# Performance work log

Hardware: AMD Instinct MI355X
Metric: run time of the kernel (lower is better)

The kernel has to match this reference:

```python
import jax, jax.numpy as jnp
import numpy as np

B, T, D = 2, 2048, 1024
H, C = 16, 64  # num_heads, head_dim
ROPE_BASE = 10000.0


def _rope(x):
    # x: [b, h, t, c]; standard rotate-half RoPE over the head dim
    t, c = x.shape[2], x.shape[3]
    inv_freq = 1.0 / (ROPE_BASE ** (jnp.arange(0, c, 2, dtype=jnp.float32) / c))  # [c/2]
    angles = jnp.arange(t, dtype=jnp.float32)[:, None] * inv_freq[None, :]        # [t, c/2]
    cos = jnp.concatenate([jnp.cos(angles), jnp.cos(angles)], axis=-1)            # [t, c]
    sin = jnp.concatenate([jnp.sin(angles), jnp.sin(angles)], axis=-1)            # [t, c]
    x1, x2 = x[..., : c // 2], x[..., c // 2 :]
    rot = jnp.concatenate([-x2, x1], axis=-1)
    return x * cos + rot * sin


def setup_inputs() -> dict:
    key = jax.random.key(0)
    ks = jax.random.split(key, 7)
    s_in = 1.0 / np.sqrt(D)
    s_attn = 1.0 / np.sqrt(H * C)
    return {
        "x": jax.random.normal(ks[0], (B, T, D), dtype=jnp.float32),
        "Wq": jax.random.normal(ks[1], (D, H * C), dtype=jnp.float32) * s_in,
        "bq": jnp.zeros((H * C,), dtype=jnp.float32),
        "Wkv": jax.random.normal(ks[2], (D, 2 * H * C), dtype=jnp.float32) * s_in,
        "bkv": jnp.zeros((2 * H * C,), dtype=jnp.float32),
        "Wo": jax.random.normal(ks[3], (H * C, D), dtype=jnp.float32) * s_attn,
        "bo": jnp.zeros((D,), dtype=jnp.float32),
    }


def reference(x, Wq, bq, Wkv, bkv, Wo, bo):
    b, t, _ = x.shape
    q = x @ Wq + bq                                  # [b, t, h*c]
    kv = x @ Wkv + bkv                               # [b, t, 2*h*c]
    k, v = jnp.split(kv, 2, axis=-1)
    # 'b t (h c) -> b h t c'
    to_heads = lambda z: z.reshape(b, t, H, C).transpose(0, 2, 1, 3)
    q, k, v = to_heads(q), to_heads(k), to_heads(v)
    q = _rope(q)
    k = _rope(k)
    scale = 1.0 / jnp.sqrt(jnp.asarray(C, dtype=q.dtype))
    scores = jnp.einsum("bhtc,bhsc->bhts", q, k) * scale   # [b, h, t, t]
    attn = jax.nn.softmax(scores, axis=-1)
    out = jnp.einsum("bhts,bhsc->bhtc", attn, v)            # [b, h, t, c]
    out = out.transpose(0, 2, 1, 3).reshape(b, t, H * C)    # 'b h t c -> b t (h c)'
    return out @ Wo + bo
```

## Files before the change

kernel.cpp:

```cpp
#include <hip/hip_runtime.h>
#include <hip/hip_bf16.h>
#include <math.h>


typedef _Float16 half8 __attribute__((ext_vector_type(8)));
typedef _Float16 half4 __attribute__((ext_vector_type(4)));
typedef float f32x4 __attribute__((ext_vector_type(4)));
typedef float f32x16 __attribute__((ext_vector_type(16)));

extern "C" __device__ float __ocml_native_exp2_f32(float);

__device__ __forceinline__ void gload16(const void* g, void* l) {
  __builtin_amdgcn_global_load_lds(
      (const __attribute__((address_space(1))) void*)g,
      (__attribute__((address_space(3))) void*)l, 16, 0, 0);
}

__global__ __launch_bounds__(256) void prep_kernel(
    const float* __restrict__ x, const float* __restrict__ Wq,
    const float* __restrict__ Wkv, const float* __restrict__ Wo,
    _Float16* __restrict__ xb, _Float16* __restrict__ Wt,
    _Float16* __restrict__ Wot, float2* __restrict__ cs)
{
  const int bid = blockIdx.x, t = threadIdx.x;
  if (bid < 2048) {
    size_t i = ((size_t)bid * 256 + t) * 8;
    const float4* p = (const float4*)(x + i);
    float4 a = p[0], b = p[1];
    half8 h;
    h[0] = (_Float16)a.x; h[1] = (_Float16)a.y; h[2] = (_Float16)a.z; h[3] = (_Float16)a.w;
    h[4] = (_Float16)b.x; h[5] = (_Float16)b.y; h[6] = (_Float16)b.z; h[7] = (_Float16)b.w;
    *(half8*)(xb + i) = h;
  } else if (bid < 6144) {
    int tt = bid - 2048;
    const float* src; _Float16* dst; int N, tk, tn;
    if (tt < 1024)      { src = Wq;  dst = Wt;                      N = 1024; tk = tt >> 5; tn = tt & 31; }
    else if (tt < 3072) { tt -= 1024; src = Wkv; dst = Wt + (size_t)1024 * 1024; N = 2048; tk = tt >> 6; tn = tt & 63; }
    else                { tt -= 3072; src = Wo;  dst = Wot;         N = 1024; tk = tt >> 5; tn = tt & 31; }
    __shared__ float tile[32][33];
    const int r = t >> 3, c4 = (t & 7) << 2;
    const float4 v = *(const float4*)(src + (size_t)(tk * 32 + r) * N + tn * 32 + c4);
    tile[r][c4 + 0] = v.x; tile[r][c4 + 1] = v.y; tile[r][c4 + 2] = v.z; tile[r][c4 + 3] = v.w;
    __syncthreads();
    half4 o;
    o[0] = (_Float16)tile[c4 + 0][r];
    o[1] = (_Float16)tile[c4 + 1][r];
    o[2] = (_Float16)tile[c4 + 2][r];
    o[3] = (_Float16)tile[c4 + 3][r];
    *(half4*)(dst + (size_t)(tn * 32 + r) * 1024 + tk * 32 + c4) = o;
  } else {
    int idx = (bid - 6144) * 256 + t;
    int tt = idx >> 5, j = idx & 31;
    float p = powf(10000.0f, (float)(2 * j) * (1.0f / 64.0f));
    float ang = (float)tt / p;
    float sn, cn;
    sincosf(ang, &sn, &cn);
    cs[idx] = make_float2(cn, sn);
  }
}

__device__ __forceinline__ void gemm_core(
    const _Float16* __restrict__ A, const _Float16* __restrict__ B,
    _Float16* __restrict__ As, _Float16* __restrict__ Bs,
    int row0, int col0, f32x4 (&acc)[4][4])
{
  const int t = threadIdx.x;
  const int l = t & 63;
  const int l15 = l & 15, lg = l >> 4;
  const int w = t >> 6;
  const int wr = (w >> 1) * 64, wc = (w & 1) * 64;
#pragma unroll
  for (int m = 0; m < 4; ++m)
#pragma unroll
    for (int n = 0; n < 4; ++n)
      acc[m][n] = (f32x4){0.f, 0.f, 0.f, 0.f};

  const int lsub = l >> 3;
  const int lcb  = (l & 7) * 16;

  for (int k0 = 0; k0 < 1024; k0 += 64) {
    __syncthreads();
#pragma unroll
    for (int i = 0; i < 4; ++i) {
      const int rb = i * 32 + w * 8;
      const int r = rb + lsub;
      const int swz = lcb ^ ((r & 7) << 4);
      gload16((const char*)A + (size_t)(row0 + r) * 2048 + (size_t)k0 * 2 + swz,
              (char*)As + rb * 128);
      gload16((const char*)B + (size_t)(col0 + r) * 2048 + (size_t)k0 * 2 + swz,
              (char*)Bs + rb * 128);
    }
    __syncthreads();
#pragma unroll
    for (int kk = 0; kk < 2; ++kk) {
      const int kb = kk * 64 + (lg << 4);
      half8 af[4], bf[4];
#pragma unroll
      for (int m = 0; m < 4; ++m) {
        const int row = wr + 16 * m + l15;
        af[m] = *(const half8*)((const char*)As + row * 128 + (kb ^ ((row & 7) << 4)));
      }
#pragma unroll
      for (int n = 0; n < 4; ++n) {
        const int col = wc + 16 * n + l15;
        bf[n] = *(const half8*)((const char*)Bs + col * 128 + (kb ^ ((col & 7) << 4)));
      }
#pragma unroll
      for (int m = 0; m < 4; ++m)
#pragma unroll
        for (int n = 0; n < 4; ++n)
          acc[m][n] = __builtin_amdgcn_mfma_f32_16x16x32_f16(af[m], bf[n], acc[m][n], 0, 0, 0);
    }
  }
}

__global__ __launch_bounds__(256) void gemm_qkv(
    const _Float16* __restrict__ xb, const _Float16* __restrict__ Wt,
    const float* __restrict__ bq, const float* __restrict__ bkv,
    const float2* __restrict__ cs,
    _Float16* __restrict__ Qb, _Float16* __restrict__ Kb, _Float16* __restrict__ Vt)
{
  __shared__ __align__(16) _Float16 As[128 * 64], Bs[128 * 64];
  f32x4 acc[4][4];
  const int row0 = blockIdx.x * 128, col0g = blockIdx.y * 128;
  const int t = threadIdx.x, l = t & 63, l15 = l & 15, lg = l >> 4, w = t >> 6;

  if (col0g < 2048) {
    gemm_core(xb, Wt, As, Bs, row0, col0g, acc);
    const int wrow = row0 + (w >> 1) * 64;
    const int ncol = col0g + (w & 1) * 64;
    const int seg = ncol >> 10;
    const int hcol = ncol & 1023;
    const int h = hcol >> 6;
    const float* bias = (seg == 0) ? bq : bkv;
    _Float16* dst = (seg == 0) ? Qb : Kb;
    const float qs = (seg == 0) ? 0.18033688011112042f : 1.0f;
    const float b0 = bias[hcol + l15],      b1 = bias[hcol + 16 + l15];
    const float b2 = bias[hcol + 32 + l15], b3 = bias[hcol + 48 + l15];
#pragma unroll
    for (int m = 0; m < 4; ++m) {
#pragma unroll
      for (int reg = 0; reg < 4; ++reg) {
        const int row = wrow + 16 * m + lg * 4 + reg;
        const int bb = row >> 11, tt = row & 2047;
        const float2 cs0 = cs[tt * 32 + l15];
        const float2 cs1 = cs[tt * 32 + 16 + l15];
        const float v0 = acc[m][0][reg] + b0;
        const float v1 = acc[m][1][reg] + b1;
        const float v2 = acc[m][2][reg] + b2;
        const float v3 = acc[m][3][reg] + b3;
        const size_t base = ((size_t)(bb * 16 + h) * 2048 + tt) * 64;
        dst[base + l15]      = (_Float16)((v0 * cs0.x - v2 * cs0.y) * qs);
        dst[base + 16 + l15] = (_Float16)((v1 * cs1.x - v3 * cs1.y) * qs);
        dst[base + 32 + l15] = (_Float16)((v2 * cs0.x + v0 * cs0.y) * qs);
        dst[base + 48 + l15] = (_Float16)((v3 * cs1.x + v1 * cs1.y) * qs);
      }
    }
  } else {
    gemm_core(Wt, xb, As, Bs, col0g, row0, acc);
    const int vcol = (col0g - 2048) + (w >> 1) * 64;
    const int tbase = row0 + (w & 1) * 64;
#pragma unroll
    for (int m = 0; m < 4; ++m) {
#pragma unroll
      for (int reg = 0; reg < 4; ++reg) {
        const int vchan = vcol + 16 * m + lg * 4 + reg;
        const float bv = bkv[1024 + vchan];
        const size_t crow = (size_t)(vchan >> 6) * 64 + (vchan & 63);
#pragma unroll
        for (int n = 0; n < 4; ++n) {
          const int tg = tbase + 16 * n + l15;
          const int bb2 = tg >> 11, tt2 = tg & 2047;
          Vt[((size_t)bb2 * 1024 + crow) * 2048 + tt2] =
              (_Float16)(acc[m][n][reg] + bv);
        }
      }
    }
  }
}

__global__ __launch_bounds__(256, 2) void attn_kernel(
    const _Float16* __restrict__ Qb, const _Float16* __restrict__ Kb,
    const _Float16* __restrict__ Vt, _Float16* __restrict__ AO)
{
  __shared__ __align__(16) _Float16 Ks[3][64 * 64], Vs[3][64 * 64];
  const int lin = blockIdx.x + (blockIdx.y << 4);
  const int xcd = lin & 7, idx = lin >> 3;
  const int bh = (xcd << 2) + (idx >> 4);
  const int qblk = (idx & 15) << 7;
  const int t = threadIdx.x, l = t & 63, l31 = l & 31, hh = l >> 5, w = t >> 6;
  const _Float16* Qg = Qb + (size_t)bh * 2048 * 64;
  const _Float16* Kg = Kb + (size_t)bh * 2048 * 64;
  const _Float16* Vg = Vt + (size_t)bh * 64 * 2048;

  const int qrow = qblk + w * 32 + l31;
  half8 qf[4];
#pragma unroll
  for (int t4 = 0; t4 < 4; ++t4)
    qf[t4] = *(const half8*)((const char*)Qg + (size_t)qrow * 128 + t4 * 32 + hh * 16);

  f32x16 oacc[2], lacc;
#pragma unroll
  for (int cc = 0; cc < 2; ++cc)
#pragma unroll
    for (int r = 0; r < 16; ++r) oacc[cc][r] = 0.f;
#pragma unroll
  for (int r = 0; r < 16; ++r) lacc[r] = 0.f;
  const half8 onesf = {(_Float16)1, (_Float16)1, (_Float16)1, (_Float16)1,
                       (_Float16)1, (_Float16)1, (_Float16)1, (_Float16)1};

  const int lsub = l >> 3;
  const int lcb  = (l & 7) * 16;

#define STAGE(s0, buf)                                                          \
  {                                                                             \
    _Pragma("unroll")                                                           \
    for (int i = 0; i < 2; ++i) {                                               \
      const int rb = w * 16 + i * 8;                                            \
      const int r = rb + lsub;                                                  \
      const int swz = lcb ^ ((r & 7) << 4);                                     \
      gload16((const char*)Kg + (size_t)((s0) + r) * 128 + swz,                 \
              (char*)Ks[buf] + rb * 128);                                       \
      gload16((const char*)Vg + (size_t)r * 4096 + (size_t)(s0) * 2 + swz,      \
              (char*)Vs[buf] + rb * 128);                                       \
    }                                                                           \
  }

  STAGE(0, 0);
  STAGE(64, 1);
  asm volatile("s_waitcnt vmcnt(4)" ::: "memory");
  __builtin_amdgcn_s_barrier();

  const int ksw = (l31 & 7) << 4;

  int cur = 0, stg = 2;
  for (int it = 0; it < 32; ++it) {
    if (it < 30) STAGE((it + 2) * 64, stg);

    f32x16 sacc[2];
#pragma unroll
    for (int s = 0; s < 2; ++s)
#pragma unroll
      for (int r = 0; r < 16; ++r) sacc[s][r] = 0.f;
#pragma unroll
    for (int s = 0; s < 2; ++s) {
      const int krow = 32 * s + l31;
#pragma unroll
      for (int t4 = 0; t4 < 4; ++t4) {
        half8 kf = *(const half8*)((const char*)Ks[cur] + krow * 128 +
                                   ((32 * t4 + 16 * hh) ^ ksw));
        sacc[s] = __builtin_amdgcn_mfma_f32_32x32x16_f16(kf, qf[t4], sacc[s], 0, 0, 0);
      }
    }

    half8 pa[4];
#pragma unroll
    for (int s = 0; s < 2; ++s) {
      unsigned wpk[8];
#pragma unroll
      for (int i = 0; i < 8; ++i) {
        const float p0 = __ocml_native_exp2_f32(sacc[s][2 * i]);
        const float p1 = __ocml_native_exp2_f32(sacc[s][2 * i + 1]);
        const auto pk = __builtin_amdgcn_cvt_pkrtz(p0, p1);
        __builtin_memcpy(&wpk[i], &pk, 4);
      }
      const auto r0 = __builtin_amdgcn_permlane32_swap(wpk[0], wpk[2], false, false);
      const auto r1 = __builtin_amdgcn_permlane32_swap(wpk[1], wpk[3], false, false);
      const auto r2 = __builtin_amdgcn_permlane32_swap(wpk[4], wpk[6], false, false);
      const auto r3 = __builtin_amdgcn_permlane32_swap(wpk[5], wpk[7], false, false);
      union { unsigned u[4]; half8 v; } lo, hi;
      lo.u[0] = r0[0]; lo.u[1] = r1[0]; lo.u[2] = r0[1]; lo.u[3] = r1[1];
      hi.u[0] = r2[0]; hi.u[1] = r3[0]; hi.u[2] = r2[1]; hi.u[3] = r3[1];
      pa[2 * s] = lo.v;
      pa[2 * s + 1] = hi.v;
    }

#pragma unroll
    for (int t4 = 0; t4 < 4; ++t4) {
      lacc = __builtin_amdgcn_mfma_f32_32x32x16_f16(pa[t4], onesf, lacc, 0, 0, 0);
#pragma unroll
      for (int cc = 0; cc < 2; ++cc) {
        const int vrow = 32 * cc + l31;
        half8 vf = *(const half8*)((const char*)Vs[cur] + vrow * 128 +
                                   ((32 * t4 + 16 * hh) ^ ksw));
        oacc[cc] = __builtin_amdgcn_mfma_f32_32x32x16_f16(pa[t4], vf, oacc[cc], 0, 0, 0);
      }
    }

    if (it < 31) {
      if (it < 30) asm volatile("s_waitcnt vmcnt(4)" ::: "memory");
      else         asm volatile("s_waitcnt vmcnt(0)" ::: "memory");
      __builtin_amdgcn_s_barrier();
    }
    cur = (cur == 2) ? 0 : cur + 1;
    stg = (stg == 2) ? 0 : stg + 1;
  }
#undef STAGE

  const int bb = bh >> 4, hd = bh & 15;
#pragma unroll
  for (int reg = 0; reg < 16; ++reg) {
    const int q = qblk + w * 32 + (reg & 3) + 8 * (reg >> 2) + 4 * hh;
    const float ir = 1.0f / lacc[reg];
    const size_t base = ((size_t)bb * 2048 + q) * 1024 + hd * 64;
    AO[base + l31]      = (_Float16)(oacc[0][reg] * ir);
    AO[base + 32 + l31] = (_Float16)(oacc[1][reg] * ir);
  }
}

__global__ __launch_bounds__(256) void gemm_out(
    const _Float16* __restrict__ AO, const _Float16* __restrict__ Wot,
    const float* __restrict__ bo, float* __restrict__ out)
{
  __shared__ __align__(16) _Float16 As[64 * 64], Bs[128 * 64];
  const int row0 = blockIdx.x * 64, col0 = blockIdx.y * 128;
  const int t = threadIdx.x, l = t & 63, l15 = l & 15, lg = l >> 4, w = t >> 6;
  const int wr = (w >> 1) * 32, wc = (w & 1) * 64;
  const int lsub = l >> 3, lcb = (l & 7) * 16;
  f32x4 acc[2][4];
#pragma unroll
  for (int m = 0; m < 2; ++m)
#pragma unroll
    for (int n = 0; n < 4; ++n)
      acc[m][n] = (f32x4){0.f, 0.f, 0.f, 0.f};

  for (int k0 = 0; k0 < 1024; k0 += 64) {
    __syncthreads();
#pragma unroll
    for (int i = 0; i < 2; ++i) {
      const int rb = w * 16 + i * 8;
      const int r = rb + lsub;
      const int swz = lcb ^ ((r & 7) << 4);
      gload16((const char*)AO + (size_t)(row0 + r) * 2048 + (size_t)k0 * 2 + swz,
              (char*)As + rb * 128);
    }
#pragma unroll
    for (int i = 0; i < 4; ++i) {
      const int rb = i * 32 + w * 8;
      const int r = rb + lsub;
      const int swz = lcb ^ ((r & 7) << 4);
      gload16((const char*)Wot + (size_t)(col0 + r) * 2048 + (size_t)k0 * 2 + swz,
              (char*)Bs + rb * 128);
    }
    __syncthreads();
#pragma unroll
    for (int kk = 0; kk < 2; ++kk) {
      const int kb = kk * 64 + (lg << 4);
      half8 af[2], bf[4];
#pragma unroll
      for (int m = 0; m < 2; ++m) {
        const int row = wr + 16 * m + l15;
        af[m] = *(const half8*)((const char*)As + row * 128 + (kb ^ ((row & 7) << 4)));
      }
#pragma unroll
      for (int n = 0; n < 4; ++n) {
        const int col = wc + 16 * n + l15;
        bf[n] = *(const half8*)((const char*)Bs + col * 128 + (kb ^ ((col & 7) << 4)));
      }
#pragma unroll
      for (int m = 0; m < 2; ++m)
#pragma unroll
        for (int n = 0; n < 4; ++n)
          acc[m][n] = __builtin_amdgcn_mfma_f32_16x16x32_f16(af[m], bf[n], acc[m][n], 0, 0, 0);
    }
  }

  const int wrow = row0 + wr, wcol = col0 + wc;
  float b[4];
#pragma unroll
  for (int n = 0; n < 4; ++n) b[n] = bo[wcol + 16 * n + l15];
#pragma unroll
  for (int m = 0; m < 2; ++m)
#pragma unroll
    for (int reg = 0; reg < 4; ++reg) {
      const int row = wrow + 16 * m + lg * 4 + reg;
#pragma unroll
      for (int n = 0; n < 4; ++n)
        out[(size_t)row * 1024 + wcol + 16 * n + l15] = acc[m][n][reg] + b[n];
    }
}

extern "C" void kernel_launch(void* const* d_in, const int* in_sizes, int n_in,
                              void* d_out, int out_size, void* d_ws, size_t ws_size,
                              hipStream_t stream)
{
  const float* x   = (const float*)d_in[0];
  const float* Wq  = (const float*)d_in[1];
  const float* bq  = (const float*)d_in[2];
  const float* Wkv = (const float*)d_in[3];
  const float* bkv = (const float*)d_in[4];
  const float* Wo  = (const float*)d_in[5];
  const float* bo  = (const float*)d_in[6];
  float* out = (float*)d_out;
  char* ws = (char*)d_ws;

  _Float16* xb  = (_Float16*)(ws);
  _Float16* Wt  = (_Float16*)(ws + 8388608);
  _Float16* Wot = (_Float16*)(ws + 14680064);
  float2*   cs  = (float2*)  (ws + 16777216);
  _Float16* Qb  = (_Float16*)(ws + 17301504);
  _Float16* Kb  = (_Float16*)(ws + 25690112);
  _Float16* Vt  = (_Float16*)(ws + 34078720);
  _Float16* AO  = (_Float16*)(ws + 42467328);

  prep_kernel<<<6400, 256, 0, stream>>>(x, Wq, Wkv, Wo, xb, Wt, Wot, cs);
  gemm_qkv<<<dim3(32, 24), 256, 0, stream>>>(xb, Wt, bq, bkv, cs, Qb, Kb, Vt);
  attn_kernel<<<dim3(16, 32), 256, 0, stream>>>(Qb, Kb, Vt, AO);
  gemm_out<<<dim3(64, 8), 256, 0, stream>>>(AO, Wot, bo, out);
}
```

Baseline: 116.3 us.

## Process two KV tiles per barrier with four-slot double-pair staging

Changes the attention K/V pipeline from a three-slot ring (one tile per iteration, prefetch distance two) to four slots processed in pairs, so each loop iteration stages the next two 64-row tiles and computes two tiles before a single barrier. This halves the number of barriers and waitcnt points in the main loop. In exchange, shared memory grows from 48KB to 64KB per block, which may limit the two-blocks-per-CU occupancy. The full vmcnt(0) wait also removes the partial overlap the old vmcnt(4) allowed.

Result: no change. 114.1 us (median of 3 runs) (-1.9%).

```diff
diff --git a/kernel.cpp b/kernel.cpp
--- a/kernel.cpp
+++ b/kernel.cpp
@@ -183,7 +183,7 @@
     const _Float16* __restrict__ Qb, const _Float16* __restrict__ Kb,
     const _Float16* __restrict__ Vt, _Float16* __restrict__ AO)
 {
-  __shared__ __align__(16) _Float16 Ks[3][64 * 64], Vs[3][64 * 64];
+  __shared__ __align__(16) _Float16 Ks[4][64 * 64], Vs[4][64 * 64];
   const int lin = blockIdx.x + (blockIdx.y << 4);
   const int xcd = lin & 7, idx = lin >> 3;
   const int bh = (xcd << 2) + (idx >> 4);
@@ -226,75 +226,81 @@
     }                                                                           \
   }
 
+  const int ksw = (l31 & 7) << 4;
+
+#define PROCESS(sb)                                                             \
+  {                                                                             \
+    f32x16 sacc[2];                                                             \
+    _Pragma("unroll")                                                           \
+    for (int s = 0; s < 2; ++s)                                                 \
+      _Pragma("unroll")                                                         \
+      for (int r = 0; r < 16; ++r) sacc[s][r] = 0.f;                            \
+    _Pragma("unroll")                                                           \
+    for (int s = 0; s < 2; ++s) {                                               \
+      const int krow = 32 * s + l31;                                            \
+      _Pragma("unroll")                                                         \
+      for (int t4 = 0; t4 < 4; ++t4) {                                          \
+        half8 kf = *(const half8*)((const char*)Ks[sb] + krow * 128 +           \
+                                   ((32 * t4 + 16 * hh) ^ ksw));                \
+        sacc[s] = __builtin_amdgcn_mfma_f32_32x32x16_f16(kf, qf[t4], sacc[s],   \
+                                                         0, 0, 0);              \
+      }                                                                         \
+    }                                                                           \
+    half8 pa[4];                                                                \
+    _Pragma("unroll")                                                           \
+    for (int s = 0; s < 2; ++s) {                                               \
+      unsigned wpk[8];                                                          \
+      _Pragma("unroll")                                                         \
+      for (int i = 0; i < 8; ++i) {                                             \
+        const float p0 = __ocml_native_exp2_f32(sacc[s][2 * i]);                \
+        const float p1 = __ocml_native_exp2_f32(sacc[s][2 * i + 1]);            \
+        const auto pk = __builtin_amdgcn_cvt_pkrtz(p0, p1);                     \
+        __builtin_memcpy(&wpk[i], &pk, 4);                                      \
+      }                                                                         \
+      const auto r0 = __builtin_amdgcn_permlane32_swap(wpk[0], wpk[2], false, false); \
+      const auto r1 = __builtin_amdgcn_permlane32_swap(wpk[1], wpk[3], false, false); \
+      const auto r2 = __builtin_amdgcn_permlane32_swap(wpk[4], wpk[6], false, false); \
+      const auto r3 = __builtin_amdgcn_permlane32_swap(wpk[5], wpk[7], false, false); \
+      union { unsigned u[4]; half8 v; } lo, hi;                                 \
+      lo.u[0] = r0[0]; lo.u[1] = r1[0]; lo.u[2] = r0[1]; lo.u[3] = r1[1];       \
+      hi.u[0] = r2[0]; hi.u[1] = r3[0]; hi.u[2] = r2[1]; hi.u[3] = r3[1];       \
+      pa[2 * s] = lo.v;                                                         \
+      pa[2 * s + 1] = hi.v;                                                     \
+    }                                                                           \
+    _Pragma("unroll")                                                           \
+    for (int t4 = 0; t4 < 4; ++t4) {                                            \
+      lacc = __builtin_amdgcn_mfma_f32_32x32x16_f16(pa[t4], onesf, lacc, 0, 0, 0); \
+      _Pragma("unroll")                                                         \
+      for (int cc = 0; cc < 2; ++cc) {                                          \
+        const int vrow = 32 * cc + l31;                                         \
+        half8 vf = *(const half8*)((const char*)Vs[sb] + vrow * 128 +           \
+                                   ((32 * t4 + 16 * hh) ^ ksw));                \
+        oacc[cc] = __builtin_amdgcn_mfma_f32_32x32x16_f16(pa[t4], vf, oacc[cc], \
+                                                          0, 0, 0);             \
+      }                                                                         \
+    }                                                                           \
+  }
+
   STAGE(0, 0);
   STAGE(64, 1);
-  asm volatile("s_waitcnt vmcnt(4)" ::: "memory");
+  asm volatile("s_waitcnt vmcnt(0)" ::: "memory");
   __builtin_amdgcn_s_barrier();
 
-  const int ksw = (l31 & 7) << 4;
-
-  int cur = 0, stg = 2;
-  for (int it = 0; it < 32; ++it) {
-    if (it < 30) STAGE((it + 2) * 64, stg);
-
-    f32x16 sacc[2];
-#pragma unroll
-    for (int s = 0; s < 2; ++s)
-#pragma unroll
-      for (int r = 0; r < 16; ++r) sacc[s][r] = 0.f;
-#pragma unroll
-    for (int s = 0; s < 2; ++s) {
-      const int krow = 32 * s + l31;
-#pragma unroll
-      for (int t4 = 0; t4 < 4; ++t4) {
-        half8 kf = *(const half8*)((const char*)Ks[cur] + krow * 128 +
-                                   ((32 * t4 + 16 * hh) ^ ksw));
-        sacc[s] = __builtin_amdgcn_mfma_f32_32x32x16_f16(kf, qf[t4], sacc[s], 0, 0, 0);
-      }
-    }
-
-    half8 pa[4];
-#pragma unroll
-    for (int s = 0; s < 2; ++s) {
-      unsigned wpk[8];
-#pragma unroll
-      for (int i = 0; i < 8; ++i) {
-        const float p0 = __ocml_native_exp2_f32(sacc[s][2 * i]);
-        const float p1 = __ocml_native_exp2_f32(sacc[s][2 * i + 1]);
-        const auto pk = __builtin_amdgcn_cvt_pkrtz(p0, p1);
-        __builtin_memcpy(&wpk[i], &pk, 4);
-      }
-      const auto r0 = __builtin_amdgcn_permlane32_swap(wpk[0], wpk[2], false, false);
-      const auto r1 = __builtin_amdgcn_permlane32_swap(wpk[1], wpk[3], false, false);
-      const auto r2 = __builtin_amdgcn_permlane32_swap(wpk[4], wpk[6], false, false);
-      const auto r3 = __builtin_amdgcn_permlane32_swap(wpk[5], wpk[7], false, false);
-      union { unsigned u[4]; half8 v; } lo, hi;
-      lo.u[0] = r0[0]; lo.u[1] = r1[0]; lo.u[2] = r0[1]; lo.u[3] = r1[1];
-      hi.u[0] = r2[0]; hi.u[1] = r3[0]; hi.u[2] = r2[1]; hi.u[3] = r3[1];
-      pa[2 * s] = lo.v;
-      pa[2 * s + 1] = hi.v;
-    }
-
-#pragma unroll
-    for (int t4 = 0; t4 < 4; ++t4) {
-      lacc = __builtin_amdgcn_mfma_f32_32x32x16_f16(pa[t4], onesf, lacc, 0, 0, 0);
-#pragma unroll
-      for (int cc = 0; cc < 2; ++cc) {
-        const int vrow = 32 * cc + l31;
-        half8 vf = *(const half8*)((const char*)Vs[cur] + vrow * 128 +
-                                   ((32 * t4 + 16 * hh) ^ ksw));
-        oacc[cc] = __builtin_amdgcn_mfma_f32_32x32x16_f16(pa[t4], vf, oacc[cc], 0, 0, 0);
-      }
-    }
-
-    if (it < 31) {
-      if (it < 30) asm volatile("s_waitcnt vmcnt(4)" ::: "memory");
-      else         asm volatile("s_waitcnt vmcnt(0)" ::: "memory");
+  for (int it = 0; it < 16; ++it) {
+    const int base = (it & 1) << 1;
+    const int sbase = (base ^ 2);
+    if (it < 15) {
+      STAGE((2 * it + 2) * 64, sbase);
+      STAGE((2 * it + 3) * 64, sbase + 1);
+    }
+    PROCESS(base);
+    PROCESS(base + 1);
+    if (it < 15) {
+      asm volatile("s_waitcnt vmcnt(0)" ::: "memory");
       __builtin_amdgcn_s_barrier();
     }
-    cur = (cur == 2) ? 0 : cur + 1;
-    stg = (stg == 2) ? 0 : stg + 1;
-  }
+  }
+#undef PROCESS
 #undef STAGE
 
   const int bb = bh >> 4, hd = bh & 15;
```
